# Kernel tuning notes

Measured on AMD Instinct MI355X. Metric: run time of the kernel, lower is better.

Reference implementation:

```python
import jax, jax.numpy as jnp
import numpy as np

D_K = 64  # module-level constant in source
NEG = -1e9


def setup_inputs() -> dict:
    key = jax.random.key(0)
    k1, k2, k3, k4 = jax.random.split(key, 4)
    B, H, S, D = 4, 16, 2048, 64
    query = jax.random.normal(k1, (B, H, S, D), dtype=jnp.float32)
    key_t = jax.random.normal(k2, (B, H, S, D), dtype=jnp.float32)
    value = jax.random.normal(k3, (B, H, S, D), dtype=jnp.float32)
    mask = jax.random.randint(k4, (B, 1, S, S), 0, 2) == 1  # bool, broadcast over heads
    return {"query": query, "key": key_t, "value": value, "mask": mask}


def reference(query, key, value, mask):
    # scores = QK^T / sqrt(d_k)   [B,H,S,S]
    scores = jnp.einsum("bhqd,bhkd->bhqk", query, key) / jnp.sqrt(jnp.float32(D_K))
    # masked_fill_(mask, -1e9)
    scores = jnp.where(mask, jnp.float32(NEG), scores)
    # non-standard: multiply masked scores by V, then log_softmax over last dim
    out = jnp.einsum("bhqk,bhkd->bhqd", scores, value)  # [B,H,S,d_v]
    return jax.nn.log_softmax(out, axis=-1)
```

## Files before the change

### kernel.cpp

```cpp
#include <hip/hip_runtime.h>
#include <hip/hip_bf16.h>


typedef __attribute__((ext_vector_type(8))) short bf16x8;
typedef __attribute__((ext_vector_type(16))) float f32x16;

#define NEGV (-1e9f)

__device__ inline unsigned cvt_bf16(float f) {
    unsigned u = __builtin_bit_cast(unsigned, f);
    u += 0x7FFFu + ((u >> 16) & 1u);
    return u >> 16;
}
__device__ inline unsigned pk_bf16(float a, float b) {
    return cvt_bf16(a) | (cvt_bf16(b) << 16);
}
__device__ inline unsigned pk_trunc(float a, float b) {
    return __builtin_amdgcn_perm(__builtin_bit_cast(unsigned, b),
                                 __builtin_bit_cast(unsigned, a), 0x07060302u);
}
__device__ inline unsigned long long shflx32_u64(unsigned long long x) {
    union { unsigned long long v; int i[2]; } u; u.v = x;
    u.i[0] = __shfl_xor(u.i[0], 32, 64);
    u.i[1] = __shfl_xor(u.i[1], 32, 64);
    return u.v;
}

__global__ __launch_bounds__(256)
void mask_pack(const int* __restrict__ M, unsigned long long* __restrict__ bitT) {
    const int lane = threadIdx.x & 63;
    const int gw   = (blockIdx.x * 256 + threadIdx.x) >> 6;
    const int nw   = (gridDim.x * 256) >> 6;
    for (int w = gw; w < 4 * 8 * 32 * 256; w += nw) {
        const int q  = w & 255;
        const int ki = (w >> 8) & 31;
        const int qt = (w >> 13) & 7;
        const int b  = w >> 16;
        const int m  = M[((size_t)(b * 2048 + qt * 256 + q)) * 2048 + ki * 64 + lane];
        const unsigned long long bal = __ballot(m != 0);
        if (lane == 0) bitT[w] = bal;
    }
}

__global__ __launch_bounds__(256, 2)
void attn_kernel(const float* __restrict__ Q, const float* __restrict__ K,
                 const float* __restrict__ V,
                 const unsigned long long* __restrict__ bitT,
                 float* __restrict__ Out) {
    __shared__ __attribute__((aligned(16))) unsigned short sS[256 * 72];
    __shared__ __attribute__((aligned(16))) unsigned short sK[2][64 * 72];
    __shared__ __attribute__((aligned(16))) unsigned short sVt[2][64 * 72];

    const int tid  = threadIdx.x;
    const int wave = tid >> 6;
    const int lane = tid & 63;
    const int half = lane >> 5;
    const int l32  = lane & 31;

    const int bid = blockIdx.x;
    const int h  = bid & 15;
    const int qt = (bid >> 4) & 7;
    const int b  = bid >> 7;
    const int bh = b * 16 + h;
    const int q0 = qt * 256;

    const float* Qb = Q + (size_t)(bh * 2048 + q0) * 64;
    const float* Kb = K + (size_t)bh * 2048 * 64;
    const float* Vb = V + (size_t)bh * 2048 * 64;
    const unsigned long long* Bt = bitT + (size_t)(b * 8 + qt) * 32 * 256
                                 + wave * 64 + half * 32 + l32;

    float4 kp[4];
    float  vp[16];
    unsigned long long mw = Bt[0];
    const int krow = tid >> 4, kc4 = tid & 15;
#pragma unroll
    for (int i = 0; i < 4; i++)
        kp[i] = *(const float4*)(Kb + (size_t)(krow + i * 16) * 64 + kc4 * 4);
#pragma unroll
    for (int i = 0; i < 2; i++) {
        const int kb = (wave * 2 + i) * 8;
#pragma unroll
        for (int j = 0; j < 8; j++)
            vp[i * 8 + j] = Vb[(size_t)(kb + j) * 64 + lane];
    }

    bf16x8 qF[2][4];
#pragma unroll
    for (int qb = 0; qb < 2; qb++) {
        const float* qr = Qb + (size_t)(wave * 64 + qb * 32 + l32) * 64 + half * 8;
#pragma unroll
        for (int dk = 0; dk < 4; dk++) {
            const float4 f0 = *(const float4*)(qr + dk * 16);
            const float4 f1 = *(const float4*)(qr + dk * 16 + 4);
            union { bf16x8 v; unsigned u[4]; } t;
            t.u[0] = pk_bf16(f0.x * 0.125f, f0.y * 0.125f);
            t.u[1] = pk_bf16(f0.z * 0.125f, f0.w * 0.125f);
            t.u[2] = pk_bf16(f1.x * 0.125f, f1.y * 0.125f);
            t.u[3] = pk_bf16(f1.z * 0.125f, f1.w * 0.125f);
            qF[qb][dk] = t.v;
        }
    }

    f32x16 Oacc[2][2];
#pragma unroll
    for (int qb = 0; qb < 2; qb++)
#pragma unroll
        for (int db = 0; db < 2; db++)
#pragma unroll
            for (int r = 0; r < 16; r++) Oacc[qb][db][r] = 0.f;

    for (int ki = 0; ki < 32; ki++) {
        const int k0  = ki * 64;
        const int cur = ki & 1;

#pragma unroll
        for (int i = 0; i < 4; i++) {
            uint2 p;
            p.x = pk_trunc(kp[i].x, kp[i].y);
            p.y = pk_trunc(kp[i].z, kp[i].w);
            *(uint2*)&sK[cur][(krow + i * 16) * 72 + kc4 * 4] = p;
        }
#pragma unroll
        for (int i = 0; i < 2; i++) {
            const int kb = (wave * 2 + i) * 8;
            uint4 p4;
            p4.x = pk_bf16(vp[i * 8 + 0], vp[i * 8 + 1]);
            p4.y = pk_bf16(vp[i * 8 + 2], vp[i * 8 + 3]);
            p4.z = pk_bf16(vp[i * 8 + 4], vp[i * 8 + 5]);
            p4.w = pk_bf16(vp[i * 8 + 6], vp[i * 8 + 7]);
            *(uint4*)&sVt[cur][lane * 72 + kb] = p4;
        }

        __syncthreads();

        unsigned long long mwN = 0;
        if (ki < 31) {
            const int kn = k0 + 64;
            mwN = Bt[(ki + 1) * 256];
#pragma unroll
            for (int i = 0; i < 4; i++)
                kp[i] = *(const float4*)(Kb + (size_t)(kn + krow + i * 16) * 64 + kc4 * 4);
#pragma unroll
            for (int i = 0; i < 2; i++) {
                const int kb = (wave * 2 + i) * 8;
#pragma unroll
                for (int j = 0; j < 8; j++)
                    vp[i * 8 + j] = Vb[(size_t)(kn + kb + j) * 64 + lane];
            }
        }

        const unsigned long long mwO = shflx32_u64(mw);
        const unsigned long long wQ0 = half ? mwO : mw;
        const unsigned long long wQ1 = half ? mw  : mwO;

#pragma unroll
        for (int jk = 0; jk < 2; jk++) {
            bf16x8 aK[4];
#pragma unroll
            for (int dk = 0; dk < 4; dk++)
                aK[dk] = *(const bf16x8*)&sK[cur][(jk * 32 + l32) * 72 + dk * 16 + half * 8];
#pragma unroll
            for (int qb = 0; qb < 2; qb++) {
                f32x16 acc;
#pragma unroll
                for (int r = 0; r < 16; r++) acc[r] = 0.f;
#pragma unroll
                for (int dk = 0; dk < 4; dk++)
                    acc = __builtin_amdgcn_mfma_f32_32x32x16_bf16(aK[dk], qF[qb][dk], acc, 0, 0, 0);
                const int qrow = wave * 64 + qb * 32 + l32;
                const unsigned b32 = (unsigned)((qb ? wQ1 : wQ0) >> (jk * 32));
#pragma unroll
                for (int rg = 0; rg < 4; rg++) {
                    const unsigned nib = b32 >> (rg * 8 + half * 4);
                    const float v0 = (nib & 1u) ? NEGV : acc[rg * 4 + 0];
                    const float v1 = (nib & 2u) ? NEGV : acc[rg * 4 + 1];
                    const float v2 = (nib & 4u) ? NEGV : acc[rg * 4 + 2];
                    const float v3 = (nib & 8u) ? NEGV : acc[rg * 4 + 3];
                    uint2 p; p.x = pk_trunc(v0, v1); p.y = pk_trunc(v2, v3);
                    *(uint2*)&sS[qrow * 72 + jk * 32 + rg * 8 + half * 4] = p;
                }
            }
        }

#pragma unroll
        for (int kkb = 0; kkb < 4; kkb++) {
            bf16x8 bV[2];
#pragma unroll
            for (int db = 0; db < 2; db++)
                bV[db] = *(const bf16x8*)&sVt[cur][(db * 32 + l32) * 72 + kkb * 16 + half * 8];
#pragma unroll
            for (int qb = 0; qb < 2; qb++) {
                const bf16x8 aS = *(const bf16x8*)&sS[(wave * 64 + qb * 32 + l32) * 72 + kkb * 16 + half * 8];
#pragma unroll
                for (int db = 0; db < 2; db++)
                    Oacc[qb][db] = __builtin_amdgcn_mfma_f32_32x32x16_bf16(aS, bV[db], Oacc[qb][db], 0, 0, 0);
            }
        }

        mw = mwN;
    }

    float* Ob = Out + (size_t)bh * 2048 * 64;
#pragma unroll
    for (int qb = 0; qb < 2; qb++) {
#pragma unroll
        for (int r = 0; r < 16; r++) {
            const float v0 = Oacc[qb][0][r], v1 = Oacc[qb][1][r];
            float mx = fmaxf(v0, v1);
#pragma unroll
            for (int off = 1; off < 32; off <<= 1)
                mx = fmaxf(mx, __shfl_xor(mx, off, 64));
            float s = __expf(v0 - mx) + __expf(v1 - mx);
#pragma unroll
            for (int off = 1; off < 32; off <<= 1)
                s += __shfl_xor(s, off, 64);
            const float lse = mx + __logf(s);
            const int qrow = q0 + wave * 64 + qb * 32 + (r & 3) + 8 * (r >> 2) + 4 * half;
            Ob[(size_t)qrow * 64 + l32]      = v0 - lse;
            Ob[(size_t)qrow * 64 + 32 + l32] = v1 - lse;
        }
    }
}

extern "C" void kernel_launch(void* const* d_in, const int* in_sizes, int n_in,
                              void* d_out, int out_size, void* d_ws, size_t ws_size,
                              hipStream_t stream) {
    const float* Q = (const float*)d_in[0];
    const float* K = (const float*)d_in[1];
    const float* V = (const float*)d_in[2];
    const int*   M = (const int*)d_in[3];
    float* Out = (float*)d_out;
    unsigned long long* bitT = (unsigned long long*)d_ws;

    mask_pack<<<dim3(4096), dim3(256), 0, stream>>>(M, bitT);
    attn_kernel<<<dim3(512), dim3(256), 0, stream>>>(Q, K, V, bitT, Out);
}
```

Baseline: 255.5 us.

## Keep score tile in registers via permlane32 swap instead of LDS round-trip

Removes the shared-memory score buffer. The masked QK^T accumulator is repacked into MFMA A-operand layout with permlane32_swap and fed straight into the PV MFMAs. The mask is now applied by initialising the accumulator with -1e9 at masked positions rather than selecting after the MFMA, which adds the dot product to -1e9 instead of replacing it. Freeing the LDS allows raising launch bounds to 3 blocks per CU, at the cost of register pressure and a slight numeric change.

```diff
diff --git a/kernel.cpp b/kernel.cpp
--- a/kernel.cpp
+++ b/kernel.cpp
@@ -18,12 +18,6 @@
 __device__ inline unsigned pk_trunc(float a, float b) {
     return __builtin_amdgcn_perm(__builtin_bit_cast(unsigned, b),
                                  __builtin_bit_cast(unsigned, a), 0x07060302u);
-}
-__device__ inline unsigned long long shflx32_u64(unsigned long long x) {
-    union { unsigned long long v; int i[2]; } u; u.v = x;
-    u.i[0] = __shfl_xor(u.i[0], 32, 64);
-    u.i[1] = __shfl_xor(u.i[1], 32, 64);
-    return u.v;
 }
 
 __global__ __launch_bounds__(256)
@@ -42,12 +36,11 @@
     }
 }
 
-__global__ __launch_bounds__(256, 2)
+__global__ __launch_bounds__(256, 3)
 void attn_kernel(const float* __restrict__ Q, const float* __restrict__ K,
                  const float* __restrict__ V,
                  const unsigned long long* __restrict__ bitT,
                  float* __restrict__ Out) {
-    __shared__ __attribute__((aligned(16))) unsigned short sS[256 * 72];
     __shared__ __attribute__((aligned(16))) unsigned short sK[2][64 * 72];
     __shared__ __attribute__((aligned(16))) unsigned short sVt[2][64 * 72];
 
@@ -111,7 +104,6 @@
             for (int r = 0; r < 16; r++) Oacc[qb][db][r] = 0.f;
 
     for (int ki = 0; ki < 32; ki++) {
-        const int k0  = ki * 64;
         const int cur = ki & 1;
 
 #pragma unroll
@@ -136,7 +128,7 @@
 
         unsigned long long mwN = 0;
         if (ki < 31) {
-            const int kn = k0 + 64;
+            const int kn = (ki + 1) * 64;
             mwN = Bt[(ki + 1) * 256];
 #pragma unroll
             for (int i = 0; i < 4; i++)
@@ -150,9 +142,14 @@
             }
         }
 
-        const unsigned long long mwO = shflx32_u64(mw);
-        const unsigned long long wQ0 = half ? mwO : mw;
-        const unsigned long long wQ1 = half ? mw  : mwO;
+        unsigned w0lo, w1lo, w0hi, w1hi;
+        {
+            union { unsigned long long v; unsigned u[2]; } mu; mu.v = mw;
+            auto rlo = __builtin_amdgcn_permlane32_swap(mu.u[0], mu.u[0], false, false);
+            auto rhi = __builtin_amdgcn_permlane32_swap(mu.u[1], mu.u[1], false, false);
+            w0lo = rlo[0]; w1lo = rlo[1];
+            w0hi = rhi[0]; w1hi = rhi[1];
+        }
 
 #pragma unroll
         for (int jk = 0; jk < 2; jk++) {
@@ -160,41 +157,48 @@
 #pragma unroll
             for (int dk = 0; dk < 4; dk++)
                 aK[dk] = *(const bf16x8*)&sK[cur][(jk * 32 + l32) * 72 + dk * 16 + half * 8];
+            bf16x8 bV[2][2];
+#pragma unroll
+            for (int p = 0; p < 2; p++)
+#pragma unroll
+                for (int db = 0; db < 2; db++)
+                    bV[p][db] = *(const bf16x8*)&sVt[cur][(db * 32 + l32) * 72 + (jk * 2 + p) * 16 + half * 8];
+
 #pragma unroll
             for (int qb = 0; qb < 2; qb++) {
+                const unsigned b32 = jk ? (qb ? w1hi : w0hi) : (qb ? w1lo : w0lo);
+                const unsigned bsh = b32 >> (half * 4);
+
                 f32x16 acc;
 #pragma unroll
-                for (int r = 0; r < 16; r++) acc[r] = 0.f;
+                for (int rg = 0; rg < 4; rg++) {
+                    const unsigned nib = bsh >> (rg * 8);
+                    acc[rg * 4 + 0] = (nib & 1u) ? NEGV : 0.f;
+                    acc[rg * 4 + 1] = (nib & 2u) ? NEGV : 0.f;
+                    acc[rg * 4 + 2] = (nib & 4u) ? NEGV : 0.f;
+                    acc[rg * 4 + 3] = (nib & 8u) ? NEGV : 0.f;
+                }
 #pragma unroll
                 for (int dk = 0; dk < 4; dk++)
                     acc = __builtin_amdgcn_mfma_f32_32x32x16_bf16(aK[dk], qF[qb][dk], acc, 0, 0, 0);
-                const int qrow = wave * 64 + qb * 32 + l32;
-                const unsigned b32 = (unsigned)((qb ? wQ1 : wQ0) >> (jk * 32));
-#pragma unroll
-                for (int rg = 0; rg < 4; rg++) {
-                    const unsigned nib = b32 >> (rg * 8 + half * 4);
-                    const float v0 = (nib & 1u) ? NEGV : acc[rg * 4 + 0];
-                    const float v1 = (nib & 2u) ? NEGV : acc[rg * 4 + 1];
-                    const float v2 = (nib & 4u) ? NEGV : acc[rg * 4 + 2];
-                    const float v3 = (nib & 8u) ? NEGV : acc[rg * 4 + 3];
-                    uint2 p; p.x = pk_trunc(v0, v1); p.y = pk_trunc(v2, v3);
-                    *(uint2*)&sS[qrow * 72 + jk * 32 + rg * 8 + half * 4] = p;
+
+#pragma unroll
+                for (int p = 0; p < 2; p++) {
+                    const unsigned P0 = pk_trunc(acc[p * 8 + 0], acc[p * 8 + 1]);
+                    const unsigned P1 = pk_trunc(acc[p * 8 + 2], acc[p * 8 + 3]);
+                    const unsigned P2 = pk_trunc(acc[p * 8 + 4], acc[p * 8 + 5]);
+                    const unsigned P3 = pk_trunc(acc[p * 8 + 6], acc[p * 8 + 7]);
+                    auto r02 = __builtin_amdgcn_permlane32_swap(P0, P2, false, false);
+                    auto r13 = __builtin_amdgcn_permlane32_swap(P1, P3, false, false);
+                    union { bf16x8 v; unsigned u[4]; } aS;
+                    aS.u[0] = (unsigned)r02[0];
+                    aS.u[1] = (unsigned)r13[0];
+                    aS.u[2] = (unsigned)r02[1];
+                    aS.u[3] = (unsigned)r13[1];
+#pragma unroll
+                    for (int db = 0; db < 2; db++)
+                        Oacc[qb][db] = __builtin_amdgcn_mfma_f32_32x32x16_bf16(aS.v, bV[p][db], Oacc[qb][db], 0, 0, 0);
                 }
-            }
-        }
-
-#pragma unroll
-        for (int kkb = 0; kkb < 4; kkb++) {
-            bf16x8 bV[2];
-#pragma unroll
-            for (int db = 0; db < 2; db++)
-                bV[db] = *(const bf16x8*)&sVt[cur][(db * 32 + l32) * 72 + kkb * 16 + half * 8];
-#pragma unroll
-            for (int qb = 0; qb < 2; qb++) {
-                const bf16x8 aS = *(const bf16x8*)&sS[(wave * 64 + qb * 32 + l32) * 72 + kkb * 16 + half * 8];
-#pragma unroll
-                for (int db = 0; db < 2; db++)
-                    Oacc[qb][db] = __builtin_amdgcn_mfma_f32_32x32x16_bf16(aS, bV[db], Oacc[qb][db], 0, 0, 0);
             }
         }
 
```

Measured after the change: 262.0 us. 2.5% more time.
